# Performance work log

Measured on AMD Instinct MI355X. Metric: run time of the kernel, lower is better.

Reference implementation:

```python
import jax, jax.numpy as jnp
import numpy as np

EPS = 1e-12  # torch F.normalize default eps

def _l2norm(x, axis=-1):
    n = jnp.linalg.norm(x, axis=axis, keepdims=True)
    return x / jnp.maximum(n, EPS)

def setup_inputs() -> dict:
    key = jax.random.key(0)
    k1, k2 = jax.random.split(key)
    query = jax.random.normal(k1, (65536, 512), dtype=jnp.float32)
    prototypes = jax.random.normal(k2, (64, 512), dtype=jnp.float32)
    return {"query": query, "prototypes": prototypes, "k": 3}

def reference(query, prototypes, k):
    # cosine similarity between queries and prototypes: [B, P]
    sim = jnp.einsum('bd,pd->bp', _l2norm(query), _l2norm(prototypes))
    k = min(int(k), prototypes.shape[0])
    weights, indices = jax.lax.top_k(sim, k)          # [B, k]
    retrieved = prototypes[indices]                   # [B, k, D]
    w = jax.nn.softmax(weights, axis=1)               # [B, k]
    return jnp.einsum('bkd,bk->bd', retrieved, w)     # [B, D]
```

## Files before the change

kernel.cpp:

```cpp
#include <hip/hip_runtime.h>
#include <math.h>

#define DIM 512
#define NP  64
#define TAU 4e-5f
#define LISTCAP 8192
#define RFB 128

#define WS_PTW   0
#define WS_PTN   131072
#define WS_BHI   262144
#define WS_BLO   327680
#define WS_INV64 393216
#define WS_CNT   393728
#define WS_LIST  393856

typedef __attribute__((ext_vector_type(8))) short bf16x8;
typedef __attribute__((ext_vector_type(4))) float f32x4;

__device__ __forceinline__ unsigned short f2bf(float f) {
  const unsigned int u = __float_as_uint(f);
  return (unsigned short)((u + 0x7FFFu + ((u >> 16) & 1u)) >> 16);
}
__device__ __forceinline__ float bf2f(unsigned short h) {
  return __uint_as_float(((unsigned int)h) << 16);
}

__device__ __forceinline__ void ins4f(float v, int idx, float& v0, float& v1,
                                      float& v2, float& v3, int& j0, int& j1,
                                      int& j2, int& j3) {
  const bool b0 = v > v0, b1 = v > v1, b2 = v > v2, b3 = v > v3;
  v3 = b2 ? v2 : (b3 ? v : v3);  j3 = b2 ? j2 : (b3 ? idx : j3);
  v2 = b1 ? v1 : (b2 ? v : v2);  j2 = b1 ? j1 : (b2 ? idx : j2);
  v1 = b0 ? v0 : (b1 ? v : v1);  j1 = b0 ? j0 : (b1 ? idx : j1);
  v0 = b0 ? v  : v0;             j0 = b0 ? idx : j0;
}

__device__ __forceinline__ void ins3d(double v, int idx, double& b0, double& b1,
                                      double& b2, int& k0, int& k1, int& k2) {
  const bool c0 = v > b0, c1 = v > b1, c2 = v > b2;
  b2 = c1 ? b1 : (c2 ? v : b2);  k2 = c1 ? k1 : (c2 ? idx : k2);
  b1 = c0 ? b0 : (c1 ? v : b1);  k1 = c0 ? k0 : (c1 ? idx : k1);
  b0 = c0 ? v  : b0;             k0 = c0 ? idx : k0;
}

__global__ __launch_bounds__(256) void prep_kernel(
    const float* __restrict__ protos, float* __restrict__ ptw,
    float* __restrict__ ptn, double* __restrict__ inv64,
    int* __restrict__ cnt) {
  if (blockIdx.x == 0 && threadIdx.x == 0) *cnt = 0;
  const int p = (blockIdx.x * 256 + threadIdx.x) >> 6;
  const int lane = threadIdx.x & 63;
  if (p >= NP) return;
  const float4* pr = (const float4*)(protos + (size_t)p * DIM);
  const float4 a = pr[lane * 2];
  const float4 b = pr[lane * 2 + 1];
  double ss = (double)a.x * a.x + (double)a.y * a.y + (double)a.z * a.z +
              (double)a.w * a.w + (double)b.x * b.x + (double)b.y * b.y +
              (double)b.z * b.z + (double)b.w * b.w;
#pragma unroll
  for (int m = 1; m < 64; m <<= 1) ss += __shfl_xor(ss, m);
  const double inv = 1.0 / fmax(sqrt(ss), 1e-12);
  if (lane == 0) inv64[p] = inv;
  const float v[8] = {a.x, a.y, a.z, a.w, b.x, b.y, b.z, b.w};
#pragma unroll
  for (int e = 0; e < 8; ++e) {
    const size_t o = (size_t)(lane * 8 + e) * NP + p;
    ptw[o] = v[e];
    ptn[o] = (float)((double)v[e] * inv);
  }
}

__global__ __launch_bounds__(64) void prep_frag_kernel(
    const float* __restrict__ ptn, unsigned short* __restrict__ bhi,
    unsigned short* __restrict__ blo) {
  const int ks = blockIdx.x >> 2;
  const int pt = blockIdx.x & 3;
  const int l = threadIdx.x;
  const int p = pt * 16 + (l & 15);
  const int k0 = ks * 32 + (l >> 4) * 8;
  const size_t base = ((size_t)(ks * 4 + pt) * 64 + l) * 8;
#pragma unroll
  for (int e = 0; e < 8; ++e) {
    const float v = ptn[(size_t)(k0 + e) * NP + p];
    const unsigned short h = f2bf(v);
    const unsigned short lo = f2bf(v - bf2f(h));
    bhi[base + e] = h;
    blo[base + e] = lo;
  }
}

__global__ __launch_bounds__(256) void sim_kernel(
    const float* __restrict__ query, const float* __restrict__ protos,
    const unsigned short* __restrict__ bhi_u, const unsigned short* __restrict__ blo_u,
    float* __restrict__ out, int* __restrict__ cnt, int* __restrict__ list) {
  __shared__ float4 wiS[4][16];

  const int t = threadIdx.x;
  const int wid = t >> 6;
  const int l = t & 63;
  const int lr = l & 15;
  const int lg = l >> 4;
  const int wr0 = blockIdx.x * 64 + wid * 16;

  const float* aq = query + (size_t)(wr0 + lr) * DIM + lg * 8;
  const bf16x8* bhp = (const bf16x8*)bhi_u;
  const bf16x8* blp = (const bf16x8*)blo_u;

  f32x4 acc[4] = {};
  float ss = 0.f;

  float4 abuf[3][2];
  bf16x8 bbuf[2][8];

#pragma unroll
  for (int s = 0; s < 3; ++s) {
    abuf[s][0] = *(const float4*)(aq + s * 32);
    abuf[s][1] = *(const float4*)(aq + s * 32 + 4);
  }
#pragma unroll
  for (int s = 0; s < 2; ++s) {
#pragma unroll
    for (int j = 0; j < 4; ++j) {
      bbuf[s][j]     = bhp[(size_t)(s * 4 + j) * 64 + l];
      bbuf[s][4 + j] = blp[(size_t)(s * 4 + j) * 64 + l];
    }
  }

#pragma unroll
  for (int ks = 0; ks < 16; ++ks) {
    const int ab = ks % 3;
    const int bb = ks & 1;
    bf16x8 ahi, alo;
    {
      const float4 a0 = abuf[ab][0];
      const float4 a1 = abuf[ab][1];
      const float av[8] = {a0.x, a0.y, a0.z, a0.w, a1.x, a1.y, a1.z, a1.w};
#pragma unroll
      for (int i = 0; i < 8; ++i) {
        const unsigned short h = f2bf(av[i]);
        ahi[i] = (short)h;
        alo[i] = (short)f2bf(av[i] - bf2f(h));
        ss += av[i] * av[i];
      }
    }
    if (ks + 3 < 16) {
      abuf[ab][0] = *(const float4*)(aq + (ks + 3) * 32);
      abuf[ab][1] = *(const float4*)(aq + (ks + 3) * 32 + 4);
    }
#pragma unroll
    for (int pt = 0; pt < 4; ++pt) {
      acc[pt] = __builtin_amdgcn_mfma_f32_16x16x32_bf16(ahi, bbuf[bb][pt],     acc[pt], 0, 0, 0);
      acc[pt] = __builtin_amdgcn_mfma_f32_16x16x32_bf16(ahi, bbuf[bb][4 + pt], acc[pt], 0, 0, 0);
      acc[pt] = __builtin_amdgcn_mfma_f32_16x16x32_bf16(alo, bbuf[bb][pt],     acc[pt], 0, 0, 0);
    }
    if (ks + 2 < 16) {
#pragma unroll
      for (int j = 0; j < 4; ++j) {
        bbuf[bb][j]     = bhp[(size_t)((ks + 2) * 4 + j) * 64 + l];
        bbuf[bb][4 + j] = blp[(size_t)((ks + 2) * 4 + j) * 64 + l];
      }
    }
  }

  ss += __shfl_xor(ss, 16);
  ss += __shfl_xor(ss, 32);

#pragma unroll
  for (int e = 0; e < 4; ++e) {
    float v0 = -1e30f, v1 = -1e30f, v2 = -1e30f, v3 = -1e30f;
    int j0 = 0, j1 = 0, j2 = 0, j3 = 0;
#pragma unroll
    for (int pt = 0; pt < 4; ++pt)
      ins4f(acc[pt][e], pt * 16 + lr, v0, v1, v2, v3, j0, j1, j2, j3);
#pragma unroll
    for (int m = 1; m <= 8; m <<= 1) {
      const float p0 = __shfl_xor(v0, m), p1 = __shfl_xor(v1, m);
      const float p2 = __shfl_xor(v2, m), p3 = __shfl_xor(v3, m);
      const int q0 = __shfl_xor(j0, m), q1 = __shfl_xor(j1, m);
      const int q2 = __shfl_xor(j2, m), q3 = __shfl_xor(j3, m);
      ins4f(p0, q0, v0, v1, v2, v3, j0, j1, j2, j3);
      ins4f(p1, q1, v0, v1, v2, v3, j0, j1, j2, j3);
      ins4f(p2, q2, v0, v1, v2, v3, j0, j1, j2, j3);
      ins4f(p3, q3, v0, v1, v2, v3, j0, j1, j2, j3);
    }
    const float ssr = __shfl(ss, lg * 4 + e);
    if (lr == e) {
      const int row = lg * 4 + e;
      const float qi = 1.0f / fmaxf(sqrtf(ssr), 1e-12f);
      const float s0 = v0 * qi, s1 = v1 * qi, s2 = v2 * qi, s3 = v3 * qi;
      const float e1 = expf(s1 - s0), e2 = expf(s2 - s0);
      const float inv = 1.0f / (1.0f + e1 + e2);
      wiS[wid][row] = make_float4(inv, e1 * inv, e2 * inv,
                                  __int_as_float(j0 | (j1 << 6) | (j2 << 12)));
      if (s2 - s3 < TAU) {
        const int pos = atomicAdd(cnt, 1);
        if (pos < LISTCAP) list[pos] = wr0 + row;
      }
    }
  }

#pragma unroll 2
  for (int r = 0; r < 16; ++r) {
    const float4 wi = wiS[wid][r];
    const int pack = __float_as_int(wi.w);
    const int i0 = pack & 63, i1 = (pack >> 6) & 63, i2 = (pack >> 12) & 63;
    const float* p0 = protos + (size_t)i0 * DIM;
    const float* p1 = protos + (size_t)i1 * DIM;
    const float* p2 = protos + (size_t)i2 * DIM;
    float* orow = out + (size_t)(wr0 + r) * DIM;
#pragma unroll
    for (int h = 0; h < 2; ++h) {
      const int col = h * 256 + l * 4;
      const float4 x = *(const float4*)(p0 + col);
      const float4 y = *(const float4*)(p1 + col);
      const float4 z = *(const float4*)(p2 + col);
      float4 res;
      res.x = wi.x * x.x + wi.y * y.x + wi.z * z.x;
      res.y = wi.x * x.y + wi.y * y.y + wi.z * z.y;
      res.z = wi.x * x.z + wi.y * y.z + wi.z * z.z;
      res.w = wi.x * x.w + wi.y * y.w + wi.z * z.w;
      *(float4*)(orow + col) = res;
    }
  }
}

__global__ __launch_bounds__(256) void refine_kernel(
    const float* __restrict__ query, const float* __restrict__ protos,
    const float* __restrict__ ptw, const double* __restrict__ inv64,
    const int* __restrict__ cnt, const int* __restrict__ list,
    float* __restrict__ out) {
  const int n = min(*cnt, LISTCAP);
  const int lane = threadIdx.x & 63;
  const int gw = blockIdx.x * 4 + (threadIdx.x >> 6);

  for (int i = gw; i < n; i += RFB * 4) {
    const int row = list[i];
    const float* q = query + (size_t)row * DIM;
    double a0 = 0.0, a1 = 0.0, a2 = 0.0, a3 = 0.0;
    float qs = 0.f;
#pragma unroll 4
    for (int k = 0; k < DIM; k += 4) {
      const float4 qv = *(const float4*)(q + k);
      a0 = fma((double)qv.x, (double)ptw[(size_t)(k + 0) * NP + lane], a0);
      a1 = fma((double)qv.y, (double)ptw[(size_t)(k + 1) * NP + lane], a1);
      a2 = fma((double)qv.z, (double)ptw[(size_t)(k + 2) * NP + lane], a2);
      a3 = fma((double)qv.w, (double)ptw[(size_t)(k + 3) * NP + lane], a3);
      qs += qv.x * qv.x + qv.y * qv.y + qv.z * qv.z + qv.w * qv.w;
    }
    const double sim = (a0 + a1 + a2 + a3) * inv64[lane];

    double b0 = sim, b1 = -1e300, b2 = -1e300;
    int k0 = lane, k1 = 0, k2 = 0;
#pragma unroll
    for (int m = 1; m <= 32; m <<= 1) {
      const double p0 = __shfl_xor(b0, m), p1 = __shfl_xor(b1, m),
                   p2 = __shfl_xor(b2, m);
      const int q0 = __shfl_xor(k0, m), q1 = __shfl_xor(k1, m),
                q2 = __shfl_xor(k2, m);
      ins3d(p0, q0, b0, b1, b2, k0, k1, k2);
      ins3d(p1, q1, b0, b1, b2, k0, k1, k2);
      ins3d(p2, q2, b0, b1, b2, k0, k1, k2);
    }
    const double qi = 1.0 / fmax(sqrt((double)qs), 1e-12);
    const double s0 = b0 * qi, s1 = b1 * qi, s2 = b2 * qi;
    const double e1 = exp(s1 - s0), e2 = exp(s2 - s0);
    const double inv = 1.0 / (1.0 + e1 + e2);
    const double w0 = inv, w1 = e1 * inv, w2 = e2 * inv;
    const float* p0r = protos + (size_t)k0 * DIM;
    const float* p1r = protos + (size_t)k1 * DIM;
    const float* p2r = protos + (size_t)k2 * DIM;
#pragma unroll
    for (int u = 0; u < 2; ++u) {
      const int col = u * 256 + lane * 4;
      const float4 x = *(const float4*)(p0r + col);
      const float4 y = *(const float4*)(p1r + col);
      const float4 z = *(const float4*)(p2r + col);
      float4 res;
      res.x = (float)(w0 * x.x + w1 * y.x + w2 * z.x);
      res.y = (float)(w0 * x.y + w1 * y.y + w2 * z.y);
      res.z = (float)(w0 * x.z + w1 * y.z + w2 * z.z);
      res.w = (float)(w0 * x.w + w1 * y.w + w2 * z.w);
      *(float4*)(out + (size_t)row * DIM + col) = res;
    }
  }
}

extern "C" void kernel_launch(void* const* d_in, const int* in_sizes, int n_in,
                              void* d_out, int out_size, void* d_ws, size_t ws_size,
                              hipStream_t stream) {
  const float* query = (const float*)d_in[0];
  const float* protos = (const float*)d_in[1];
  float* out = (float*)d_out;
  float* ptw = (float*)((char*)d_ws + WS_PTW);
  float* ptn = (float*)((char*)d_ws + WS_PTN);
  unsigned short* bhi = (unsigned short*)((char*)d_ws + WS_BHI);
  unsigned short* blo = (unsigned short*)((char*)d_ws + WS_BLO);
  double* inv64 = (double*)((char*)d_ws + WS_INV64);
  int* cnt = (int*)((char*)d_ws + WS_CNT);
  int* list = (int*)((char*)d_ws + WS_LIST);

  const int nrows = in_sizes[0] / DIM;

  hipLaunchKernelGGL(prep_kernel, dim3(16), dim3(256), 0, stream,
                     protos, ptw, ptn, inv64, cnt);
  hipLaunchKernelGGL(prep_frag_kernel, dim3(64), dim3(64), 0, stream,
                     ptn, bhi, blo);
  hipLaunchKernelGGL(sim_kernel, dim3(nrows / 64), dim3(256), 0, stream,
                     query, protos, bhi, blo, out, cnt, list);
  hipLaunchKernelGGL(refine_kernel, dim3(RFB), dim3(256), 0, stream,
                     query, protos, ptw, inv64, cnt, list, out);
}
```

Measured before the change: 130.5 us.

## Stage prototype hi fragments in LDS and double rows per block

The sim kernel now copies the full bf16 high-part prototype fragment array (64 KB) into shared memory once per block and reads it from LDS in the MFMA loop. Only the low-part fragments are still streamed from global memory. Blocks grow to 512 threads covering 128 rows, with launch bounds asking for 4 blocks per CU. The prep stage also drops the intermediate normalized-prototype buffer and builds the fragments directly from the raw prototypes and inverse norms. This is meant to cut repeated global/L2 traffic for the B operand, at the cost of a large LDS footprint that may limit occupancy, plus a startup copy and barrier in every block.

```diff
diff --git a/kernel.cpp b/kernel.cpp
--- a/kernel.cpp
+++ b/kernel.cpp
@@ -3,17 +3,17 @@
 
 #define DIM 512
 #define NP  64
+#define RPB 128
 #define TAU 4e-5f
 #define LISTCAP 8192
 #define RFB 128
 
 #define WS_PTW   0
-#define WS_PTN   131072
-#define WS_BHI   262144
-#define WS_BLO   327680
-#define WS_INV64 393216
-#define WS_CNT   393728
-#define WS_LIST  393856
+#define WS_BHI   131072
+#define WS_BLO   196608
+#define WS_INV64 262144
+#define WS_CNT   262656
+#define WS_LIST  262784
 
 typedef __attribute__((ext_vector_type(8))) short bf16x8;
 typedef __attribute__((ext_vector_type(4))) float f32x4;
@@ -46,8 +46,7 @@
 
 __global__ __launch_bounds__(256) void prep_kernel(
     const float* __restrict__ protos, float* __restrict__ ptw,
-    float* __restrict__ ptn, double* __restrict__ inv64,
-    int* __restrict__ cnt) {
+    double* __restrict__ inv64, int* __restrict__ cnt) {
   if (blockIdx.x == 0 && threadIdx.x == 0) *cnt = 0;
   const int p = (blockIdx.x * 256 + threadIdx.x) >> 6;
   const int lane = threadIdx.x & 63;
@@ -64,54 +63,62 @@
   if (lane == 0) inv64[p] = inv;
   const float v[8] = {a.x, a.y, a.z, a.w, b.x, b.y, b.z, b.w};
 #pragma unroll
-  for (int e = 0; e < 8; ++e) {
-    const size_t o = (size_t)(lane * 8 + e) * NP + p;
-    ptw[o] = v[e];
-    ptn[o] = (float)((double)v[e] * inv);
-  }
+  for (int e = 0; e < 8; ++e)
+    ptw[(size_t)(lane * 8 + e) * NP + p] = v[e];
 }
 
 __global__ __launch_bounds__(64) void prep_frag_kernel(
-    const float* __restrict__ ptn, unsigned short* __restrict__ bhi,
-    unsigned short* __restrict__ blo) {
+    const float* __restrict__ protos, const double* __restrict__ inv64,
+    unsigned short* __restrict__ bhi, unsigned short* __restrict__ blo) {
   const int ks = blockIdx.x >> 2;
   const int pt = blockIdx.x & 3;
   const int l = threadIdx.x;
   const int p = pt * 16 + (l & 15);
   const int k0 = ks * 32 + (l >> 4) * 8;
+  const double inv = inv64[p];
   const size_t base = ((size_t)(ks * 4 + pt) * 64 + l) * 8;
 #pragma unroll
   for (int e = 0; e < 8; ++e) {
-    const float v = ptn[(size_t)(k0 + e) * NP + p];
+    const float v = (float)((double)protos[(size_t)p * DIM + k0 + e] * inv);
     const unsigned short h = f2bf(v);
-    const unsigned short lo = f2bf(v - bf2f(h));
     bhi[base + e] = h;
-    blo[base + e] = lo;
-  }
-}
-
-__global__ __launch_bounds__(256) void sim_kernel(
+    blo[base + e] = f2bf(v - bf2f(h));
+  }
+}
+
+__global__ __launch_bounds__(512, 4) void sim_kernel(
     const float* __restrict__ query, const float* __restrict__ protos,
     const unsigned short* __restrict__ bhi_u, const unsigned short* __restrict__ blo_u,
     float* __restrict__ out, int* __restrict__ cnt, int* __restrict__ list) {
-  __shared__ float4 wiS[4][16];
+  __shared__ __align__(16) short BHI[16 * 4 * 64 * 8];
+  __shared__ float4 wiS[8][16];
 
   const int t = threadIdx.x;
   const int wid = t >> 6;
   const int l = t & 63;
   const int lr = l & 15;
   const int lg = l >> 4;
-  const int wr0 = blockIdx.x * 64 + wid * 16;
+  const int wr0 = blockIdx.x * RPB + wid * 16;
+
+  {
+    const float4* gs = (const float4*)bhi_u;
+    float4 tmp[8];
+#pragma unroll
+    for (int i = 0; i < 8; ++i) tmp[i] = gs[i * 512 + t];
+#pragma unroll
+    for (int i = 0; i < 8; ++i)
+      *(float4*)&BHI[(i * 512 + t) * 8] = tmp[i];
+  }
+  __syncthreads();
 
   const float* aq = query + (size_t)(wr0 + lr) * DIM + lg * 8;
-  const bf16x8* bhp = (const bf16x8*)bhi_u;
   const bf16x8* blp = (const bf16x8*)blo_u;
 
   f32x4 acc[4] = {};
   float ss = 0.f;
 
   float4 abuf[3][2];
-  bf16x8 bbuf[2][8];
+  bf16x8 lbuf[2][4];
 
 #pragma unroll
   for (int s = 0; s < 3; ++s) {
@@ -119,13 +126,10 @@
     abuf[s][1] = *(const float4*)(aq + s * 32 + 4);
   }
 #pragma unroll
-  for (int s = 0; s < 2; ++s) {
-#pragma unroll
-    for (int j = 0; j < 4; ++j) {
-      bbuf[s][j]     = bhp[(size_t)(s * 4 + j) * 64 + l];
-      bbuf[s][4 + j] = blp[(size_t)(s * 4 + j) * 64 + l];
-    }
-  }
+  for (int s = 0; s < 2; ++s)
+#pragma unroll
+    for (int j = 0; j < 4; ++j)
+      lbuf[s][j] = blp[(size_t)(s * 4 + j) * 64 + l];
 
 #pragma unroll
   for (int ks = 0; ks < 16; ++ks) {
@@ -148,18 +152,20 @@
       abuf[ab][0] = *(const float4*)(aq + (ks + 3) * 32);
       abuf[ab][1] = *(const float4*)(aq + (ks + 3) * 32 + 4);
     }
+    bf16x8 bh[4];
+#pragma unroll
+    for (int pt = 0; pt < 4; ++pt)
+      bh[pt] = *(const bf16x8*)&BHI[((ks * 4 + pt) * 64 + l) * 8];
 #pragma unroll
     for (int pt = 0; pt < 4; ++pt) {
-      acc[pt] = __builtin_amdgcn_mfma_f32_16x16x32_bf16(ahi, bbuf[bb][pt],     acc[pt], 0, 0, 0);
-      acc[pt] = __builtin_amdgcn_mfma_f32_16x16x32_bf16(ahi, bbuf[bb][4 + pt], acc[pt], 0, 0, 0);
-      acc[pt] = __builtin_amdgcn_mfma_f32_16x16x32_bf16(alo, bbuf[bb][pt],     acc[pt], 0, 0, 0);
+      acc[pt] = __builtin_amdgcn_mfma_f32_16x16x32_bf16(ahi, bh[pt],       acc[pt], 0, 0, 0);
+      acc[pt] = __builtin_amdgcn_mfma_f32_16x16x32_bf16(ahi, lbuf[bb][pt], acc[pt], 0, 0, 0);
+      acc[pt] = __builtin_amdgcn_mfma_f32_16x16x32_bf16(alo, bh[pt],       acc[pt], 0, 0, 0);
     }
     if (ks + 2 < 16) {
 #pragma unroll
-      for (int j = 0; j < 4; ++j) {
-        bbuf[bb][j]     = bhp[(size_t)((ks + 2) * 4 + j) * 64 + l];
-        bbuf[bb][4 + j] = blp[(size_t)((ks + 2) * 4 + j) * 64 + l];
-      }
+      for (int j = 0; j < 4; ++j)
+        lbuf[bb][j] = blp[(size_t)((ks + 2) * 4 + j) * 64 + l];
     }
   }
 
@@ -293,7 +299,6 @@
   const float* protos = (const float*)d_in[1];
   float* out = (float*)d_out;
   float* ptw = (float*)((char*)d_ws + WS_PTW);
-  float* ptn = (float*)((char*)d_ws + WS_PTN);
   unsigned short* bhi = (unsigned short*)((char*)d_ws + WS_BHI);
   unsigned short* blo = (unsigned short*)((char*)d_ws + WS_BLO);
   double* inv64 = (double*)((char*)d_ws + WS_INV64);
@@ -303,10 +308,10 @@
   const int nrows = in_sizes[0] / DIM;
 
   hipLaunchKernelGGL(prep_kernel, dim3(16), dim3(256), 0, stream,
-                     protos, ptw, ptn, inv64, cnt);
+                     protos, ptw, inv64, cnt);
   hipLaunchKernelGGL(prep_frag_kernel, dim3(64), dim3(64), 0, stream,
-                     ptn, bhi, blo);
-  hipLaunchKernelGGL(sim_kernel, dim3(nrows / 64), dim3(256), 0, stream,
+                     protos, inv64, bhi, blo);
+  hipLaunchKernelGGL(sim_kernel, dim3(nrows / RPB), dim3(512), 0, stream,
                      query, protos, bhi, blo, out, cnt, list);
   hipLaunchKernelGGL(refine_kernel, dim3(RFB), dim3(256), 0, stream,
                      query, protos, ptw, inv64, cnt, list, out);
```

Result: slower. 154.4 us (+18.3%).
